# Kernel tuning notes

Measured on AMD Instinct MI355X. Metric: run time of the kernel, lower is better.

## Reference

```python
import jax, jax.numpy as jnp
import numpy as np

EPS = 1e-06
N_HEADS = 16


def elu_feature_map(x):
    return jax.nn.elu(x) + 1.0


def setup_inputs() -> dict:
    key = jax.random.key(0)
    ks = jax.random.split(key, 5)
    B, S, D = 4, 4096, 1024
    scale = 1.0 / np.sqrt(D)
    x = jax.random.normal(ks[0], (B, S, D), dtype=jnp.float32)
    Wq = jax.random.normal(ks[1], (D, D), dtype=jnp.float32) * scale
    Wk = jax.random.normal(ks[2], (D, D), dtype=jnp.float32) * scale
    Wv = jax.random.normal(ks[3], (D, D), dtype=jnp.float32) * scale
    Wo = jax.random.normal(ks[4], (D, D), dtype=jnp.float32) * scale
    return {"x": x, "Wq": Wq, "Wk": Wk, "Wv": Wv, "Wo": Wo}


def reference(x, Wq, Wk, Wv, Wo):
    B, S, D = x.shape
    H = N_HEADS
    hd = D // H
    # nn.Linear(bias=False): y = x @ W.T
    q = (x @ Wq.T).reshape(B, S, H, hd)
    k = (x @ Wk.T).reshape(B, S, H, hd)
    v = (x @ Wv.T).reshape(B, S, H, hd)
    q = elu_feature_map(q)
    k = elu_feature_map(k)
    KV = jnp.einsum('bshd,bshe->bhde', k, v)          # [B,H,hd,hd]
    out = jnp.einsum('bshd,bhde->bshe', q, KV)        # [B,S,H,hd]
    k_sum = k.sum(axis=1)                             # [B,H,hd]
    z = jnp.einsum('bshd,bhd->bsh', q, k_sum)[..., None]
    out = out / (z + EPS)
    out = out.reshape(B, S, D)
    return out @ Wo.T
```

## Files before the change

kernel.cpp:

```cpp
#include <hip/hip_runtime.h>
#include <hip/hip_bf16.h>

#define BB 4
#define SS 4096
#define DD 1024
#define HH 16
#define HD 64
#define MM (BB * SS)
#define KK DD
#define NN DD

typedef __bf16 bf16x8 __attribute__((ext_vector_type(8)));
typedef float f32x4 __attribute__((ext_vector_type(4)));

typedef __attribute__((address_space(3))) void lds_void_t;
typedef const __attribute__((address_space(1))) void glb_void_t;

__global__ __launch_bounds__(256)
void cvt_f32_bf16(const float* __restrict__ in, __hip_bfloat16* __restrict__ out, int n4) {
    int i = blockIdx.x * 256 + threadIdx.x;
    if (i >= n4) return;
    float4 v = ((const float4*)in)[i];
    union { __hip_bfloat16 h[4]; uint2 u; } r;
    r.h[0] = __float2bfloat16(v.x);
    r.h[1] = __float2bfloat16(v.y);
    r.h[2] = __float2bfloat16(v.z);
    r.h[3] = __float2bfloat16(v.w);
    ((uint2*)out)[i] = r.u;
}

__global__ __launch_bounds__(256, 2)
void gemm_qkv(const __hip_bfloat16* __restrict__ X,
              const __hip_bfloat16* __restrict__ Wq,
              const __hip_bfloat16* __restrict__ Wk,
              const __hip_bfloat16* __restrict__ Wv,
              __hip_bfloat16* __restrict__ Qo,
              __hip_bfloat16* __restrict__ Ko,
              __hip_bfloat16* __restrict__ Vo)
{
    __shared__ __align__(16) __hip_bfloat16 sA[128][32];
    __shared__ __align__(16) __hip_bfloat16 sBq[64][32];
    __shared__ __align__(16) __hip_bfloat16 sBk[64][32];
    __shared__ __align__(16) __hip_bfloat16 sBv[64][32];

    const int l     = blockIdx.x;
    const int chunk = l >> 8;
    const int idx   = l & 255;
    const int n0 = ((chunk & 1) * 8 + (idx & 7)) * 64;
    const int m0 = ((chunk >> 1) * 32 + (idx >> 3)) * 128;

    const int t    = threadIdx.x;
    const int lane = t & 63;
    const int wv   = t >> 6;
    const int wm   = (wv >> 1) * 64;
    const int wn   = (wv & 1) * 32;
    const int lr   = lane & 15;
    const int lq   = lane >> 4;

    f32x4 aq[4][2], ak[4][2], av[4][2];
    #pragma unroll
    for (int i = 0; i < 4; i++)
        #pragma unroll
        for (int j = 0; j < 2; j++) {
            aq[i][j] = (f32x4){0.f, 0.f, 0.f, 0.f};
            ak[i][j] = (f32x4){0.f, 0.f, 0.f, 0.f};
            av[i][j] = (f32x4){0.f, 0.f, 0.f, 0.f};
        }

    for (int kk = 0; kk < KK; kk += 32) {
        #pragma unroll
        for (int i = 0; i < 2; i++) {
            int s = i * 256 + t;
            int r = s >> 2, c = (s & 3) * 8;
            __builtin_amdgcn_global_load_lds(
                (glb_void_t*)&X[(size_t)(m0 + r) * KK + kk + c],
                (lds_void_t*)&sA[r][c], 16, 0, 0);
        }
        {
            int r = t >> 2, c = (t & 3) * 8;
            size_t go = (size_t)(n0 + r) * KK + kk + c;
            __builtin_amdgcn_global_load_lds((glb_void_t*)&Wq[go], (lds_void_t*)&sBq[r][c], 16, 0, 0);
            __builtin_amdgcn_global_load_lds((glb_void_t*)&Wk[go], (lds_void_t*)&sBk[r][c], 16, 0, 0);
            __builtin_amdgcn_global_load_lds((glb_void_t*)&Wv[go], (lds_void_t*)&sBv[r][c], 16, 0, 0);
        }
        __syncthreads();

        bf16x8 af[4], bq[2], bk[2], bv[2];
        #pragma unroll
        for (int i = 0; i < 4; i++)
            af[i] = *(const bf16x8*)(&sA[wm + i * 16 + lr][lq * 8]);
        #pragma unroll
        for (int j = 0; j < 2; j++) {
            bq[j] = *(const bf16x8*)(&sBq[wn + j * 16 + lr][lq * 8]);
            bk[j] = *(const bf16x8*)(&sBk[wn + j * 16 + lr][lq * 8]);
            bv[j] = *(const bf16x8*)(&sBv[wn + j * 16 + lr][lq * 8]);
        }
        #pragma unroll
        for (int i = 0; i < 4; i++)
            #pragma unroll
            for (int j = 0; j < 2; j++) {
                aq[i][j] = __builtin_amdgcn_mfma_f32_16x16x32_bf16(af[i], bq[j], aq[i][j], 0, 0, 0);
                ak[i][j] = __builtin_amdgcn_mfma_f32_16x16x32_bf16(af[i], bk[j], ak[i][j], 0, 0, 0);
                av[i][j] = __builtin_amdgcn_mfma_f32_16x16x32_bf16(af[i], bv[j], av[i][j], 0, 0, 0);
            }
        __syncthreads();
    }

    #pragma unroll
    for (int i = 0; i < 4; i++) {
        #pragma unroll
        for (int j = 0; j < 2; j++) {
            #pragma unroll
            for (int r = 0; r < 4; r++) {
                size_t off = (size_t)(m0 + wm + i * 16 + lq * 4 + r) * NN
                           + (n0 + wn + j * 16 + lr);
                float vq = aq[i][j][r];
                float vk = ak[i][j][r];
                Qo[off] = __float2bfloat16(vq > 0.f ? vq + 1.f : __expf(vq));
                Ko[off] = __float2bfloat16(vk > 0.f ? vk + 1.f : __expf(vk));
                Vo[off] = __float2bfloat16(av[i][j][r]);
            }
        }
    }
}

__global__ __launch_bounds__(256)
void gemm_out(const __hip_bfloat16* __restrict__ X,
              const __hip_bfloat16* __restrict__ W,
              float* __restrict__ Cf)
{
    __shared__ __align__(16) __hip_bfloat16 sA[128][32];
    __shared__ __align__(16) __hip_bfloat16 sB[128][32];

    const int l     = blockIdx.x;
    const int chunk = l >> 8;
    const int n0 = (l & 7) * 128;
    const int m0 = (chunk * 32 + ((l >> 3) & 31)) * 128;

    const int t    = threadIdx.x;
    const int lane = t & 63;
    const int wv   = t >> 6;
    const int wm   = (wv >> 1) * 64;
    const int wn   = (wv & 1) * 64;
    const int lrow = lane & 15;
    const int lq   = lane >> 4;

    f32x4 acc[4][4];
    #pragma unroll
    for (int i = 0; i < 4; i++)
        #pragma unroll
        for (int j = 0; j < 4; j++)
            acc[i][j] = (f32x4){0.f, 0.f, 0.f, 0.f};

    for (int kk = 0; kk < KK; kk += 32) {
        #pragma unroll
        for (int i = 0; i < 2; i++) {
            int li = (t + i * 256) * 8;
            int r  = li >> 5;
            int c  = li & 31;
            __builtin_amdgcn_global_load_lds(
                (glb_void_t*)&X[(size_t)(m0 + r) * KK + kk + c],
                (lds_void_t*)&sA[r][c], 16, 0, 0);
            __builtin_amdgcn_global_load_lds(
                (glb_void_t*)&W[(size_t)(n0 + r) * KK + kk + c],
                (lds_void_t*)&sB[r][c], 16, 0, 0);
        }
        __syncthreads();

        bf16x8 af[4], bfv[4];
        #pragma unroll
        for (int i = 0; i < 4; i++) {
            af[i]  = *(const bf16x8*)(&sA[wm + i * 16 + lrow][lq * 8]);
            bfv[i] = *(const bf16x8*)(&sB[wn + i * 16 + lrow][lq * 8]);
        }
        #pragma unroll
        for (int i = 0; i < 4; i++)
            #pragma unroll
            for (int j = 0; j < 4; j++)
                acc[i][j] = __builtin_amdgcn_mfma_f32_16x16x32_bf16(af[i], bfv[j], acc[i][j], 0, 0, 0);
        __syncthreads();
    }

    #pragma unroll
    for (int i = 0; i < 4; i++)
        #pragma unroll
        for (int j = 0; j < 4; j++)
            #pragma unroll
            for (int r = 0; r < 4; r++) {
                int row = m0 + wm + i * 16 + lq * 4 + r;
                int col = n0 + wn + j * 16 + lrow;
                Cf[(size_t)row * NN + col] = acc[i][j][r];
            }
}

#define KV_SPLIT 8
__global__ __launch_bounds__(256)
void kv_mfma(const __hip_bfloat16* __restrict__ Kt,
             const __hip_bfloat16* __restrict__ Vt,
             float* __restrict__ KVp)
{
    __shared__ __hip_bfloat16 sK[128 * 64];
    __shared__ __hip_bfloat16 sV[128 * 64];
    __shared__ float sRed[65 * 66];

    const int bh = blockIdx.x;
    const int b  = bh >> 4;
    const int h  = bh & 15;
    const int sp = blockIdx.y;
    const int t  = threadIdx.x;
    const int lane = t & 63;
    const int wv = t >> 6;
    const int lr = lane & 15;
    const int lq = lane >> 4;
    const int s0blk = sp * (SS / KV_SPLIT);

    const __hip_bfloat16* kbase = Kt + ((size_t)b * SS + s0blk) * DD + h * HD;
    const __hip_bfloat16* vbase = Vt + ((size_t)b * SS + s0blk) * DD + h * HD;

    f32x4 acc[4][4];
    f32x4 ksacc[4];
    #pragma unroll
    for (int i = 0; i < 4; i++) {
        ksacc[i] = (f32x4){0.f, 0.f, 0.f, 0.f};
        #pragma unroll
        for (int j = 0; j < 4; j++)
            acc[i][j] = (f32x4){0.f, 0.f, 0.f, 0.f};
    }

    bf16x8 ones;
    #pragma unroll
    for (int j = 0; j < 8; j++) ones[j] = (__bf16)1.0f;

    for (int sc = 0; sc < 4; sc++) {
        const int srow0 = sc * 128;
        #pragma unroll
        for (int i = 0; i < 4; i++) {
            int slot = i * 256 + t;
            int r = slot >> 3;
            int o = (t & 7) ^ ((r >> 3) & 3);
            size_t goff = (size_t)(srow0 + r) * DD + o * 8;
            __builtin_amdgcn_global_load_lds(
                (glb_void_t*)(kbase + goff),
                (lds_void_t*)((char*)sK + slot * 16), 16, 0, 0);
            __builtin_amdgcn_global_load_lds(
                (glb_void_t*)(vbase + goff),
                (lds_void_t*)((char*)sV + slot * 16), 16, 0, 0);
        }
        __syncthreads();

        bf16x8 ak[4], bv[4];
        #pragma unroll
        for (int i = 0; i < 4; i++) {
            #pragma unroll
            for (int j = 0; j < 8; j++) {
                int r = wv * 32 + lq * 8 + j;
                int d = i * 16 + lr;
                int idx = r * 64 + (((d >> 3) ^ lq) << 3) + (d & 7);
                ak[i][j] = ((const __bf16*)sK)[idx];
                bv[i][j] = ((const __bf16*)sV)[idx];
            }
        }
        #pragma unroll
        for (int i = 0; i < 4; i++) {
            #pragma unroll
            for (int j = 0; j < 4; j++)
                acc[i][j] = __builtin_amdgcn_mfma_f32_16x16x32_bf16(ak[i], bv[j], acc[i][j], 0, 0, 0);
            ksacc[i] = __builtin_amdgcn_mfma_f32_16x16x32_bf16(ak[i], ones, ksacc[i], 0, 0, 0);
        }
        __syncthreads();
    }

    for (int w = 0; w < 4; w++) {
        if (wv == w) {
            #pragma unroll
            for (int i = 0; i < 4; i++) {
                #pragma unroll
                for (int j = 0; j < 4; j++) {
                    float* p = &sRed[(j * 16 + lr) * 66 + i * 16 + lq * 4];
                    if (w == 0) {
                        #pragma unroll
                        for (int r = 0; r < 4; r++) p[r] = acc[i][j][r];
                    } else {
                        #pragma unroll
                        for (int r = 0; r < 4; r++) p[r] += acc[i][j][r];
                    }
                }
                if (lr == 0) {
                    float* p = &sRed[64 * 66 + i * 16 + lq * 4];
                    if (w == 0) {
                        #pragma unroll
                        for (int r = 0; r < 4; r++) p[r] = ksacc[i][r];
                    } else {
                        #pragma unroll
                        for (int r = 0; r < 4; r++) p[r] += ksacc[i][r];
                    }
                }
            }
        }
        __syncthreads();
    }

    float* outp = KVp + (size_t)(sp * 64 + bh) * (65 * 64);
    #pragma unroll
    for (int i = 0; i < 17; i++) {
        int idx = i * 256 + t;
        if (idx < 65 * 64) {
            int e = idx >> 6, d = idx & 63;
            outp[idx] = sRed[e * 66 + d];
        }
    }
}

__global__ __launch_bounds__(256)
void kv_reduce(const float* __restrict__ KVp,
               __hip_bfloat16* __restrict__ KVt,
               float* __restrict__ KS)
{
    const int bh = blockIdx.x;
    const int t  = threadIdx.x;
    #pragma unroll
    for (int i = 0; i < 16; i++) {
        int idx = i * 256 + t;
        float s = 0.f;
        #pragma unroll
        for (int sp = 0; sp < KV_SPLIT; sp++)
            s += KVp[((size_t)(sp * 64 + bh) * 65) * 64 + idx];
        KVt[(size_t)bh * 4096 + idx] = __float2bfloat16(s);
    }
    if (t < 64) {
        float s = 0.f;
        #pragma unroll
        for (int sp = 0; sp < KV_SPLIT; sp++)
            s += KVp[((size_t)(sp * 64 + bh) * 65 + 64) * 64 + t];
        KS[bh * 64 + t] = s;
    }
}

__global__ __launch_bounds__(256)
void attn_mfma(const __hip_bfloat16* __restrict__ Q,
               const __hip_bfloat16* __restrict__ KVt,
               const float* __restrict__ KS,
               __hip_bfloat16* __restrict__ O)
{
    const int bh = blockIdx.x;
    const int b  = bh >> 4;
    const int h  = bh & 15;
    const int s0 = blockIdx.y * 128;
    const int t  = threadIdx.x;
    const int lane = t & 63;
    const int wv = t >> 6;

    __shared__ __align__(16) __hip_bfloat16 sQ[128][72];
    __shared__ __align__(16) __hip_bfloat16 sKVt[64][72];
    __shared__ float sKS[64];
    __shared__ float sZ[128];

    {
        const float4* kvp = (const float4*)(KVt + (size_t)bh * 4096);
        #pragma unroll
        for (int i = 0; i < 2; i++) {
            int c = i * 256 + t;
            *(float4*)(&sKVt[c >> 3][(c & 7) * 8]) = kvp[c];
        }
        if (t < 64) sKS[t] = KS[bh * 64 + t];
    }
    {
        const __hip_bfloat16* qp = Q + ((size_t)b * SS + s0) * DD + h * HD;
        int r  = t >> 1;
        int c0 = (t & 1) * 32;
        #pragma unroll
        for (int i = 0; i < 32; i += 8)
            *(float4*)(&sQ[r][c0 + i]) = *(const float4*)(qp + (size_t)r * DD + c0 + i);
    }
    __syncthreads();

    if (t < 128) {
        float z = 0.f;
        #pragma unroll
        for (int d8 = 0; d8 < 64; d8 += 8) {
            bf16x8 qv = *(const bf16x8*)(&sQ[t][d8]);
            #pragma unroll
            for (int j = 0; j < 8; j++) z += (float)qv[j] * sKS[d8 + j];
        }
        sZ[t] = 1.f / (z + 1e-6f);
    }

    const int lr = lane & 15;
    const int lq = lane >> 4;
    f32x4 acc[2][4];
    #pragma unroll
    for (int i = 0; i < 2; i++)
        #pragma unroll
        for (int j = 0; j < 4; j++)
            acc[i][j] = (f32x4){0.f, 0.f, 0.f, 0.f};

    bf16x8 af[2][2], bfv[4][2];
    #pragma unroll
    for (int ks = 0; ks < 2; ks++) {
        #pragma unroll
        for (int i = 0; i < 2; i++)
            af[i][ks] = *(const bf16x8*)(&sQ[wv * 32 + i * 16 + lr][lq * 8 + ks * 32]);
        #pragma unroll
        for (int j = 0; j < 4; j++)
            bfv[j][ks] = *(const bf16x8*)(&sKVt[j * 16 + lr][lq * 8 + ks * 32]);
    }
    #pragma unroll
    for (int i = 0; i < 2; i++)
        #pragma unroll
        for (int j = 0; j < 4; j++) {
            acc[i][j] = __builtin_amdgcn_mfma_f32_16x16x32_bf16(af[i][0], bfv[j][0], acc[i][j], 0, 0, 0);
            acc[i][j] = __builtin_amdgcn_mfma_f32_16x16x32_bf16(af[i][1], bfv[j][1], acc[i][j], 0, 0, 0);
        }
    __syncthreads();

    __hip_bfloat16* op = O + ((size_t)b * SS + s0) * DD + h * HD;
    #pragma unroll
    for (int i = 0; i < 2; i++)
        #pragma unroll
        for (int j = 0; j < 4; j++)
            #pragma unroll
            for (int r = 0; r < 4; r++) {
                int row = wv * 32 + i * 16 + lq * 4 + r;
                int col = j * 16 + lr;
                op[(size_t)row * DD + col] = __float2bfloat16(acc[i][j][r] * sZ[row]);
            }
}

extern "C" void kernel_launch(void* const* d_in, const int* in_sizes, int n_in,
                              void* d_out, int out_size, void* d_ws, size_t ws_size,
                              hipStream_t stream) {
    const float* x  = (const float*)d_in[0];
    const float* Wq = (const float*)d_in[1];
    const float* Wk = (const float*)d_in[2];
    const float* Wv = (const float*)d_in[3];
    const float* Wo = (const float*)d_in[4];
    float* out = (float*)d_out;

    char* ws = (char*)d_ws;
    const size_t XB_BYTES = (size_t)MM * KK * 2;
    const size_t WB_BYTES = (size_t)NN * KK * 2;
    __hip_bfloat16* xb  = (__hip_bfloat16*)(ws);
    __hip_bfloat16* wqb = (__hip_bfloat16*)(ws + XB_BYTES);
    __hip_bfloat16* wkb = (__hip_bfloat16*)(ws + XB_BYTES + WB_BYTES);
    __hip_bfloat16* wvb = (__hip_bfloat16*)(ws + XB_BYTES + 2 * WB_BYTES);
    __hip_bfloat16* wob = (__hip_bfloat16*)(ws + XB_BYTES + 3 * WB_BYTES);
    __hip_bfloat16* qb  = (__hip_bfloat16*)(ws + XB_BYTES + 4 * WB_BYTES);
    __hip_bfloat16* kb  = (__hip_bfloat16*)(ws + 2 * XB_BYTES + 4 * WB_BYTES);
    __hip_bfloat16* vb  = (__hip_bfloat16*)(ws + 3 * XB_BYTES + 4 * WB_BYTES);
    __hip_bfloat16* KVt = (__hip_bfloat16*)(ws + 4 * XB_BYTES + 4 * WB_BYTES);
    float*          KS  = (float*)(ws + 4 * XB_BYTES + 4 * WB_BYTES + 524288);
    float* KVp = (float*)(ws);
    __hip_bfloat16* ab = xb;

    const int XN = MM * KK;
    const int WN = NN * KK;

    cvt_f32_bf16<<<XN / 4 / 256, 256, 0, stream>>>(x,  xb,  XN / 4);
    cvt_f32_bf16<<<WN / 4 / 256, 256, 0, stream>>>(Wq, wqb, WN / 4);
    cvt_f32_bf16<<<WN / 4 / 256, 256, 0, stream>>>(Wk, wkb, WN / 4);
    cvt_f32_bf16<<<WN / 4 / 256, 256, 0, stream>>>(Wv, wvb, WN / 4);
    cvt_f32_bf16<<<WN / 4 / 256, 256, 0, stream>>>(Wo, wob, WN / 4);

    gemm_qkv<<<2048, 256, 0, stream>>>(xb, wqb, wkb, wvb, qb, kb, vb);

    kv_mfma<<<dim3(BB * HH, KV_SPLIT), 256, 0, stream>>>(kb, vb, KVp);
    kv_reduce<<<BB * HH, 256, 0, stream>>>(KVp, KVt, KS);

    attn_mfma<<<dim3(BB * HH, SS / 128), 256, 0, stream>>>(qb, KVt, KS, ab);

    gemm_out<<<1024, 256, 0, stream>>>(ab, wob, out);
}
```

Before: 376.2 us.

## Replace QKV and output GEMMs with 256x256 double-buffered swizzled MFMA kernel

Replaces the separate QKV and output GEMM kernels with one templated 256x256-tile, 512-thread GEMM. It uses XOR-swizzled LDS, double-buffered async global-to-LDS loads with explicit vmcnt waits, phased barriers and setprio around the MFMA bursts. The QKV pass treats Wq/Wk/Wv as one contiguous 3072-row weight matrix, selects the output buffer by column block and applies the ELU feature map to the Q and K blocks. This relies on wqb, wkb, wvb and qb, kb, vb each being contiguous in the workspace. The aim is more operand reuse per LDS load and better overlap of memory traffic with MFMA work, at the cost of high register and LDS pressure and fragile hand-written wait counts.

New measurement: 347.7 us. 7.6% less time.

```diff
diff --git a/kernel.cpp b/kernel.cpp
--- a/kernel.cpp
+++ b/kernel.cpp
@@ -29,168 +29,156 @@
     ((uint2*)out)[i] = r.u;
 }
 
-__global__ __launch_bounds__(256, 2)
-void gemm_qkv(const __hip_bfloat16* __restrict__ X,
-              const __hip_bfloat16* __restrict__ Wq,
-              const __hip_bfloat16* __restrict__ Wk,
-              const __hip_bfloat16* __restrict__ Wv,
-              __hip_bfloat16* __restrict__ Qo,
-              __hip_bfloat16* __restrict__ Ko,
-              __hip_bfloat16* __restrict__ Vo)
+#define RD_A(dst, idx)                                                                   \
+    dst[0] = *(const bf16x8*)(sAb + ((idx) * 16 + lr) * 128 + ((lq * 16) ^ swz));        \
+    dst[1] = *(const bf16x8*)(sAb + ((idx) * 16 + lr) * 128 + (((64) + lq * 16) ^ swz));
+
+#define PH_WAIT                                                 \
+    __builtin_amdgcn_s_barrier();                               \
+    asm volatile("s_waitcnt lgkmcnt(0)" ::: "memory");          \
+    __builtin_amdgcn_sched_barrier(0);
+
+#define MFMA2(i0, i1, va, vb)                                                                         \
+    __builtin_amdgcn_s_setprio(1);                                                                    \
+    _Pragma("unroll")                                                                                 \
+    for (int j = 0; j < 4; ++j) {                                                                     \
+        acc[i0][j] = __builtin_amdgcn_mfma_f32_16x16x32_bf16(va[0], bfr[j][0], acc[i0][j], 0, 0, 0);  \
+        acc[i0][j] = __builtin_amdgcn_mfma_f32_16x16x32_bf16(va[1], bfr[j][1], acc[i0][j], 0, 0, 0);  \
+        acc[i1][j] = __builtin_amdgcn_mfma_f32_16x16x32_bf16(vb[0], bfr[j][0], acc[i1][j], 0, 0, 0);  \
+        acc[i1][j] = __builtin_amdgcn_mfma_f32_16x16x32_bf16(vb[1], bfr[j][1], acc[i1][j], 0, 0, 0);  \
+    }                                                                                                 \
+    __builtin_amdgcn_s_setprio(0);
+
+template<int MODE>
+__global__ __launch_bounds__(512, 2)
+void gemm256(const __hip_bfloat16* __restrict__ Ain,
+             const __hip_bfloat16* __restrict__ Bin,
+             __hip_bfloat16* __restrict__ Obf,
+             float* __restrict__ Of32)
 {
-    __shared__ __align__(16) __hip_bfloat16 sA[128][32];
-    __shared__ __align__(16) __hip_bfloat16 sBq[64][32];
-    __shared__ __align__(16) __hip_bfloat16 sBk[64][32];
-    __shared__ __align__(16) __hip_bfloat16 sBv[64][32];
-
-    const int l     = blockIdx.x;
-    const int chunk = l >> 8;
-    const int idx   = l & 255;
-    const int n0 = ((chunk & 1) * 8 + (idx & 7)) * 64;
-    const int m0 = ((chunk >> 1) * 32 + (idx >> 3)) * 128;
-
-    const int t    = threadIdx.x;
-    const int lane = t & 63;
-    const int wv   = t >> 6;
-    const int wm   = (wv >> 1) * 64;
-    const int wn   = (wv & 1) * 32;
-    const int lr   = lane & 15;
-    const int lq   = lane >> 4;
-
-    f32x4 aq[4][2], ak[4][2], av[4][2];
-    #pragma unroll
-    for (int i = 0; i < 4; i++)
-        #pragma unroll
-        for (int j = 0; j < 2; j++) {
-            aq[i][j] = (f32x4){0.f, 0.f, 0.f, 0.f};
-            ak[i][j] = (f32x4){0.f, 0.f, 0.f, 0.f};
-            av[i][j] = (f32x4){0.f, 0.f, 0.f, 0.f};
-        }
-
-    for (int kk = 0; kk < KK; kk += 32) {
-        #pragma unroll
-        for (int i = 0; i < 2; i++) {
-            int s = i * 256 + t;
-            int r = s >> 2, c = (s & 3) * 8;
-            __builtin_amdgcn_global_load_lds(
-                (glb_void_t*)&X[(size_t)(m0 + r) * KK + kk + c],
-                (lds_void_t*)&sA[r][c], 16, 0, 0);
-        }
-        {
-            int r = t >> 2, c = (t & 3) * 8;
-            size_t go = (size_t)(n0 + r) * KK + kk + c;
-            __builtin_amdgcn_global_load_lds((glb_void_t*)&Wq[go], (lds_void_t*)&sBq[r][c], 16, 0, 0);
-            __builtin_amdgcn_global_load_lds((glb_void_t*)&Wk[go], (lds_void_t*)&sBk[r][c], 16, 0, 0);
-            __builtin_amdgcn_global_load_lds((glb_void_t*)&Wv[go], (lds_void_t*)&sBv[r][c], 16, 0, 0);
-        }
-        __syncthreads();
-
-        bf16x8 af[4], bq[2], bk[2], bv[2];
-        #pragma unroll
-        for (int i = 0; i < 4; i++)
-            af[i] = *(const bf16x8*)(&sA[wm + i * 16 + lr][lq * 8]);
-        #pragma unroll
-        for (int j = 0; j < 2; j++) {
-            bq[j] = *(const bf16x8*)(&sBq[wn + j * 16 + lr][lq * 8]);
-            bk[j] = *(const bf16x8*)(&sBk[wn + j * 16 + lr][lq * 8]);
-            bv[j] = *(const bf16x8*)(&sBv[wn + j * 16 + lr][lq * 8]);
-        }
-        #pragma unroll
-        for (int i = 0; i < 4; i++)
-            #pragma unroll
-            for (int j = 0; j < 2; j++) {
-                aq[i][j] = __builtin_amdgcn_mfma_f32_16x16x32_bf16(af[i], bq[j], aq[i][j], 0, 0, 0);
-                ak[i][j] = __builtin_amdgcn_mfma_f32_16x16x32_bf16(af[i], bk[j], ak[i][j], 0, 0, 0);
-                av[i][j] = __builtin_amdgcn_mfma_f32_16x16x32_bf16(af[i], bv[j], av[i][j], 0, 0, 0);
+    __shared__ __align__(16) __hip_bfloat16 sA[2][2][128 * 64];
+    __shared__ __align__(16) __hip_bfloat16 sB[2][2][128 * 64];
+
+    const int nwg = gridDim.x;
+    const int bid = blockIdx.x;
+    const int s   = (bid & 7) * (nwg >> 3) + (bid >> 3);
+    const int m0  = (s & 63) << 8;
+    const int n0  = (s >> 6) << 8;
+
+    const int t      = threadIdx.x;
+    const int lane   = t & 63;
+    const int w      = t >> 6;
+    const int warp_m = w >> 2;
+    const int warp_n = w & 3;
+    const int halfB  = warp_n >> 1;
+    const int bn     = (warp_n & 1) << 6;
+    const int lr     = lane & 15;
+    const int lq     = lane >> 4;
+    const int swz    = (lr & 7) << 4;
+
+    const int trow = t >> 3;
+    const int tcb  = (((t & 7) ^ ((t >> 3) & 7)) << 4);
+
+    auto stage = [&](int ht) {
+        if (ht >= 64) return;
+        const int ts   = ht >> 2;
+        const int kind = ht & 3;
+        const int half = kind & 1;
+        #pragma unroll
+        for (int i = 0; i < 2; ++i) {
+            const int row = i * 64 + trow;
+            if (kind >= 2) {
+                __builtin_amdgcn_global_load_lds(
+                    (glb_void_t*)(Ain + (size_t)(m0 + half * 128 + row) * 1024 + ts * 64 + (tcb >> 1)),
+                    (lds_void_t*)(&sA[ts & 1][half][(i * 512 + t) * 8]), 16, 0, 0);
+            } else {
+                __builtin_amdgcn_global_load_lds(
+                    (glb_void_t*)(Bin + (size_t)(n0 + half * 128 + row) * 1024 + ts * 64 + (tcb >> 1)),
+                    (lds_void_t*)(&sB[ts & 1][half][(i * 512 + t) * 8]), 16, 0, 0);
             }
-        __syncthreads();
-    }
-
-    #pragma unroll
-    for (int i = 0; i < 4; i++) {
-        #pragma unroll
-        for (int j = 0; j < 2; j++) {
-            #pragma unroll
-            for (int r = 0; r < 4; r++) {
-                size_t off = (size_t)(m0 + wm + i * 16 + lq * 4 + r) * NN
-                           + (n0 + wn + j * 16 + lr);
-                float vq = aq[i][j][r];
-                float vk = ak[i][j][r];
-                Qo[off] = __float2bfloat16(vq > 0.f ? vq + 1.f : __expf(vq));
-                Ko[off] = __float2bfloat16(vk > 0.f ? vk + 1.f : __expf(vk));
-                Vo[off] = __float2bfloat16(av[i][j][r]);
-            }
-        }
-    }
-}
-
-__global__ __launch_bounds__(256)
-void gemm_out(const __hip_bfloat16* __restrict__ X,
-              const __hip_bfloat16* __restrict__ W,
-              float* __restrict__ Cf)
-{
-    __shared__ __align__(16) __hip_bfloat16 sA[128][32];
-    __shared__ __align__(16) __hip_bfloat16 sB[128][32];
-
-    const int l     = blockIdx.x;
-    const int chunk = l >> 8;
-    const int n0 = (l & 7) * 128;
-    const int m0 = (chunk * 32 + ((l >> 3) & 31)) * 128;
-
-    const int t    = threadIdx.x;
-    const int lane = t & 63;
-    const int wv   = t >> 6;
-    const int wm   = (wv >> 1) * 64;
-    const int wn   = (wv & 1) * 64;
-    const int lrow = lane & 15;
-    const int lq   = lane >> 4;
-
-    f32x4 acc[4][4];
-    #pragma unroll
-    for (int i = 0; i < 4; i++)
-        #pragma unroll
-        for (int j = 0; j < 4; j++)
+        }
+    };
+
+    f32x4 acc[8][4];
+    #pragma unroll
+    for (int i = 0; i < 8; ++i)
+        #pragma unroll
+        for (int j = 0; j < 4; ++j)
             acc[i][j] = (f32x4){0.f, 0.f, 0.f, 0.f};
 
-    for (int kk = 0; kk < KK; kk += 32) {
-        #pragma unroll
-        for (int i = 0; i < 2; i++) {
-            int li = (t + i * 256) * 8;
-            int r  = li >> 5;
-            int c  = li & 31;
-            __builtin_amdgcn_global_load_lds(
-                (glb_void_t*)&X[(size_t)(m0 + r) * KK + kk + c],
-                (lds_void_t*)&sA[r][c], 16, 0, 0);
-            __builtin_amdgcn_global_load_lds(
-                (glb_void_t*)&W[(size_t)(n0 + r) * KK + kk + c],
-                (lds_void_t*)&sB[r][c], 16, 0, 0);
-        }
-        __syncthreads();
-
-        bf16x8 af[4], bfv[4];
-        #pragma unroll
-        for (int i = 0; i < 4; i++) {
-            af[i]  = *(const bf16x8*)(&sA[wm + i * 16 + lrow][lq * 8]);
-            bfv[i] = *(const bf16x8*)(&sB[wn + i * 16 + lrow][lq * 8]);
-        }
-        #pragma unroll
-        for (int i = 0; i < 4; i++)
-            #pragma unroll
-            for (int j = 0; j < 4; j++)
-                acc[i][j] = __builtin_amdgcn_mfma_f32_16x16x32_bf16(af[i], bfv[j], acc[i][j], 0, 0, 0);
-        __syncthreads();
-    }
-
-    #pragma unroll
-    for (int i = 0; i < 4; i++)
-        #pragma unroll
-        for (int j = 0; j < 4; j++)
-            #pragma unroll
-            for (int r = 0; r < 4; r++) {
-                int row = m0 + wm + i * 16 + lq * 4 + r;
-                int col = n0 + wn + j * 16 + lrow;
-                Cf[(size_t)row * NN + col] = acc[i][j][r];
-            }
+    stage(0); stage(1); stage(2); stage(3);
+    asm volatile("s_waitcnt vmcnt(4)" ::: "memory");
+    stage(4); stage(5); stage(6);
+    asm volatile("s_waitcnt vmcnt(6)" ::: "memory");
+    __builtin_amdgcn_s_barrier();
+
+    #pragma unroll 2
+    for (int kt = 0; kt < 16; ++kt) {
+        const char* sAb = (const char*)&sA[kt & 1][warp_m][0];
+        const char* sBb = (const char*)&sB[kt & 1][halfB][0];
+        bf16x8 bfr[4][2];
+        bf16x8 a0[2], a1[2], a2[2], a3[2], a4[2], a5[2], a6[2], a7[2];
+
+        #pragma unroll
+        for (int j = 0; j < 4; ++j) {
+            bfr[j][0] = *(const bf16x8*)(sBb + (bn + j * 16 + lr) * 128 + ((lq * 16) ^ swz));
+            bfr[j][1] = *(const bf16x8*)(sBb + (bn + j * 16 + lr) * 128 + ((64 + lq * 16) ^ swz));
+        }
+        RD_A(a0, 0); RD_A(a1, 1);
+        stage(4 * kt + 7);
+        PH_WAIT;
+        MFMA2(0, 1, a0, a1);
+        __builtin_amdgcn_s_barrier();
+
+        RD_A(a2, 2); RD_A(a3, 3); RD_A(a4, 4); RD_A(a5, 5);
+        stage(4 * kt + 8);
+        PH_WAIT;
+        MFMA2(2, 3, a2, a3);
+        __builtin_amdgcn_s_barrier();
+
+        RD_A(a6, 6); RD_A(a7, 7);
+        stage(4 * kt + 9);
+        PH_WAIT;
+        MFMA2(4, 5, a4, a5);
+        __builtin_amdgcn_s_barrier();
+
+        stage(4 * kt + 10);
+        __builtin_amdgcn_s_barrier();
+        MFMA2(6, 7, a6, a7);
+        if (kt < 14)       { asm volatile("s_waitcnt vmcnt(6)" ::: "memory"); }
+        else if (kt == 14) { asm volatile("s_waitcnt vmcnt(0)" ::: "memory"); }
+        __builtin_amdgcn_s_barrier();
+    }
+
+    if constexpr (MODE == 0) {
+        const int wsel = n0 >> 10;
+        const int nb   = n0 & 1023;
+        __hip_bfloat16* Op = Obf + (size_t)wsel * ((size_t)MM * KK);
+        const bool doelu = (wsel < 2);
+        #pragma unroll
+        for (int i = 0; i < 8; ++i)
+            #pragma unroll
+            for (int j = 0; j < 4; ++j)
+                #pragma unroll
+                for (int r = 0; r < 4; ++r) {
+                    const int row = m0 + warp_m * 128 + i * 16 + lq * 4 + r;
+                    const int col = nb + warp_n * 64 + j * 16 + lr;
+                    float v = acc[i][j][r];
+                    if (doelu) v = (v > 0.f) ? v + 1.f : __expf(v);
+                    Op[(size_t)row * 1024 + col] = __float2bfloat16(v);
+                }
+    } else {
+        #pragma unroll
+        for (int i = 0; i < 8; ++i)
+            #pragma unroll
+            for (int j = 0; j < 4; ++j)
+                #pragma unroll
+                for (int r = 0; r < 4; ++r) {
+                    const int row = m0 + warp_m * 128 + i * 16 + lq * 4 + r;
+                    const int col = n0 + warp_n * 64 + j * 16 + lr;
+                    Of32[(size_t)row * 1024 + col] = acc[i][j][r];
+                }
+    }
 }
 
 #define KV_SPLIT 8
@@ -461,12 +449,12 @@
     cvt_f32_bf16<<<WN / 4 / 256, 256, 0, stream>>>(Wv, wvb, WN / 4);
     cvt_f32_bf16<<<WN / 4 / 256, 256, 0, stream>>>(Wo, wob, WN / 4);
 
-    gemm_qkv<<<2048, 256, 0, stream>>>(xb, wqb, wkb, wvb, qb, kb, vb);
+    gemm256<0><<<768, 512, 0, stream>>>(xb, wqb, qb, nullptr);
 
     kv_mfma<<<dim3(BB * HH, KV_SPLIT), 256, 0, stream>>>(kb, vb, KVp);
     kv_reduce<<<BB * HH, 256, 0, stream>>>(KVp, KVt, KS);
 
     attn_mfma<<<dim3(BB * HH, SS / 128), 256, 0, stream>>>(qb, KVt, KS, ab);
 
-    gemm_out<<<1024, 256, 0, stream>>>(ab, wob, out);
-}
+    gemm256<1><<<256, 512, 0, stream>>>(ab, wob, nullptr, out);
+}
```
